# Performance work log

Measured on AMD Instinct MI355X. Metric: run time of the kernel, lower is better.

The kernel has to match this reference:

```python
import jax, jax.numpy as jnp
import numpy as np
from jax import lax

B, T = 32, 256
VOCAB, WDIM, MDIM = 50000, 300, 50
HID, NLAYERS, NCLASSES = 512, 2, 3


def _init(key, shape, scale):
    return (jax.random.normal(key, shape, dtype=jnp.float32) * scale)


def setup_inputs() -> dict:
    key = jax.random.key(0)
    ks = jax.random.split(key, 20)
    inputs_seq = jax.random.randint(ks[0], (B, T), 0, VOCAB, dtype=jnp.int32)
    masks = jax.random.randint(ks[1], (B, T), 0, 2, dtype=jnp.int32)
    length = jax.random.randint(ks[2], (B, 1), T // 2, T + 1, dtype=jnp.int32)
    embedding = _init(ks[3], (VOCAB, WDIM), 0.1)
    mask_embedding = _init(ks[4], (2, MDIM), 0.1)
    transition = _init(ks[5], (2, 2), 1.0)
    d_in0 = WDIM + MDIM          # 350
    d_in1 = 2 * HID              # 1024
    w_fw0 = _init(ks[6], (d_in0 + HID, 4 * HID), 0.02)
    b_fw0 = jnp.zeros((4 * HID,), jnp.float32)
    w_bw0 = _init(ks[7], (d_in0 + HID, 4 * HID), 0.02)
    b_bw0 = jnp.zeros((4 * HID,), jnp.float32)
    w_fw1 = _init(ks[8], (d_in1 + HID, 4 * HID), 0.02)
    b_fw1 = jnp.zeros((4 * HID,), jnp.float32)
    w_bw1 = _init(ks[9], (d_in1 + HID, 4 * HID), 0.02)
    b_bw1 = jnp.zeros((4 * HID,), jnp.float32)
    crf_w = _init(ks[10], (2 * HID, 2), 0.02)
    crf_b = jnp.zeros((2,), jnp.float32)
    logits_w = _init(ks[11], (2 * HID, NCLASSES), 0.02)
    logits_b = jnp.zeros((NCLASSES,), jnp.float32)
    return dict(inputs_seq=inputs_seq, masks=masks, length=length,
                embedding=embedding, mask_embedding=mask_embedding,
                transition=transition,
                w_fw0=w_fw0, b_fw0=b_fw0, w_bw0=w_bw0, b_bw0=b_bw0,
                w_fw1=w_fw1, b_fw1=b_fw1, w_bw1=w_bw1, b_bw1=b_bw1,
                crf_w=crf_w, crf_b=crf_b, logits_w=logits_w, logits_b=logits_b)


def _lstm_scan(x, length, W, b):
    """TF LSTMCell (gate order i, j, f, o; forget_bias=1.0) over time.
    Outputs are zeroed and state held past sequence_length (dynamic_rnn semantics)."""
    Bb, Tt, _ = x.shape
    H = W.shape[1] // 4
    zero = jnp.zeros((Bb, H), x.dtype)

    def step(carry, inp):
        h, c = carry
        xt, t = inp
        z = jnp.concatenate([xt, h], axis=-1) @ W + b
        i, j, f, o = jnp.split(z, 4, axis=-1)
        c_new = jax.nn.sigmoid(f + 1.0) * c + jax.nn.sigmoid(i) * jnp.tanh(j)
        h_new = jax.nn.sigmoid(o) * jnp.tanh(c_new)
        m = (t < length)[:, None]
        c = jnp.where(m, c_new, c)
        h = jnp.where(m, h_new, h)
        out = jnp.where(m, h_new, 0.0)
        return (h, c), out

    _, ys = lax.scan(step, (zero, zero), (x.transpose(1, 0, 2), jnp.arange(Tt)))
    return ys.transpose(1, 0, 2)  # [B,T,H]


def _reverse_seq(x, length):
    """tf.reverse_sequence along time: reverse first `length` steps, keep rest."""
    Tt = x.shape[1]
    t = jnp.arange(Tt)[None, :]
    L = length[:, None]
    idx = jnp.where(t < L, L - 1 - t, t)  # [B,T]
    return jnp.take_along_axis(x, idx[:, :, None], axis=1)


def _forward(inputs_seq, masks, length, embedding, mask_embedding, transition,
             lstm_params, crf_w, crf_b, logits_w, logits_b):
    length = length.reshape(-1)  # tf.squeeze
    emb = embedding[inputs_seq]          # [B,T,WDIM]
    memb = mask_embedding[masks]         # [B,T,MDIM]
    out = jnp.concatenate([emb, memb], axis=-1)
    for (wf, bf, wb, bb) in lstm_params:
        fw = _lstm_scan(out, length, wf, bf)
        bw = _reverse_seq(_lstm_scan(_reverse_seq(out, length), length, wb, bb), length)
        out = jnp.concatenate([fw, bw], axis=-1)  # [B,T,2H]

    # CRF forward probabilities over 2 tags
    e = out @ crf_w + crf_b              # [B,T,2] emission scores
    Tt = e.shape[1]
    alpha0 = e[:, 0]

    def crf_step(alpha, inp):
        et, t = inp
        new = jax.nn.logsumexp(alpha[:, :, None] + transition[None], axis=1) + et
        m = (t < length)[:, None]
        alpha = jnp.where(m, new, alpha)
        p = jnp.where(m, jax.nn.softmax(alpha, axis=-1), 0.0)
        return alpha, p

    _, probs_rest = lax.scan(crf_step, alpha0,
                             (e[:, 1:].transpose(1, 0, 2), jnp.arange(1, Tt)))
    p0 = jnp.where((length > 0)[:, None], jax.nn.softmax(alpha0, axis=-1), 0.0)
    probs = jnp.concatenate([p0[None], probs_rest], axis=0).transpose(1, 0, 2)  # [B,T,2]

    crf_out = probs[:, :, -1][:, None, :]            # [B,1,T]
    sentiment_vector = crf_out @ out                  # [B,1,2H]
    logits = jax.nn.softmax(sentiment_vector @ logits_w + logits_b, axis=-1)
    return logits  # [B,1,NCLASSES]


def reference(inputs_seq, masks, length, embedding, mask_embedding, transition,
              w_fw0, b_fw0, w_bw0, b_bw0, w_fw1, b_fw1, w_bw1, b_bw1,
              crf_w, crf_b, logits_w, logits_b):
    lstm_params = [(w_fw0, b_fw0, w_bw0, b_bw0), (w_fw1, b_fw1, w_bw1, b_bw1)]
    return _forward(inputs_seq, masks, length, embedding, mask_embedding,
                    transition, lstm_params, crf_w, crf_b, logits_w, logits_b)
```

## Files before the change

kernel.cpp:

```cpp
#include <hip/hip_runtime.h>
#include <hip/hip_bf16.h>
#include <cstdint>
#include <cstddef>

#define BB 32
#define TT 256
#define HID 512

typedef __attribute__((ext_vector_type(8))) short short8v;
typedef __attribute__((ext_vector_type(4))) float float4v;
typedef __attribute__((ext_vector_type(4))) unsigned int uint4v;

__device__ __forceinline__ float bf2f(unsigned short u) {
  return __uint_as_float(((unsigned int)u) << 16);
}
__device__ __forceinline__ unsigned short f2bf(float f) {
  unsigned int x = __float_as_uint(f);
  x += 0x7fffu + ((x >> 16) & 1u);
  return (unsigned short)(x >> 16);
}

__device__ __forceinline__ void stg1_cohere(float* p, float v) {
  asm volatile("global_store_dword %0, %1, off sc0 sc1"
               :: "v"(p), "v"(v) : "memory");
}
__device__ __forceinline__ void ldg4u_cohere_issue(uint4v& d, const unsigned short* p) {
  asm volatile("global_load_dwordx4 %0, %1, off sc0 sc1"
               : "=v"(d) : "v"(p) : "memory");
}
__device__ __forceinline__ void wait_vm0() {
  asm volatile("s_waitcnt vmcnt(0)" ::: "memory");
  __builtin_amdgcn_sched_barrier(0);
}

__global__ __launch_bounds__(256) void prep_all(
    const float* __restrict__ w_fw0, const float* __restrict__ w_bw0,
    const float* __restrict__ w_fw1, const float* __restrict__ w_bw1,
    unsigned short* __restrict__ wxt0f, unsigned short* __restrict__ wxt0b,
    unsigned short* __restrict__ wxt1f, unsigned short* __restrict__ wxt1b,
    unsigned short* __restrict__ whT0f, unsigned short* __restrict__ whT0b,
    unsigned short* __restrict__ whT1f, unsigned short* __restrict__ whT1b,
    const int* __restrict__ ids, const int* __restrict__ msk,
    const float* __restrict__ emb, const float* __restrict__ memb,
    unsigned short* __restrict__ x0b,
    float* __restrict__ zero_base)
{
  __shared__ float tile[64][65];
  int blk = blockIdx.x;
  int tid = threadIdx.x;
  if (blk < 2432) {
    const float* W; unsigned short* dst; int Kreal, Kpad, base;
    if (blk < 192)       { W = w_fw0; dst = wxt0f; Kreal = 350;  Kpad = 384;  base = 0; }
    else if (blk < 384)  { W = w_bw0; dst = wxt0b; Kreal = 350;  Kpad = 384;  base = 192; }
    else if (blk < 896)  { W = w_fw1; dst = wxt1f; Kreal = 1024; Kpad = 1024; base = 384; }
    else if (blk < 1408) { W = w_bw1; dst = wxt1b; Kreal = 1024; Kpad = 1024; base = 896; }
    else if (blk < 1664) { W = w_fw0 + (size_t)350 * 2048;  dst = whT0f; Kreal = 512; Kpad = 512; base = 1408; }
    else if (blk < 1920) { W = w_bw0 + (size_t)350 * 2048;  dst = whT0b; Kreal = 512; Kpad = 512; base = 1664; }
    else if (blk < 2176) { W = w_fw1 + (size_t)1024 * 2048; dst = whT1f; Kreal = 512; Kpad = 512; base = 1920; }
    else                 { W = w_bw1 + (size_t)1024 * 2048; dst = whT1b; Kreal = 512; Kpad = 512; base = 2176; }
    int rel = blk - base;
    int n0 = (rel & 31) * 64;
    int k0 = (rel >> 5) * 64;
#pragma unroll
    for (int i = 0; i < 4; ++i) {
      int e = tid + 256 * i;
      int r = e >> 4, c4 = (e & 15) * 4;
      float4 v = make_float4(0.f, 0.f, 0.f, 0.f);
      if (k0 + r < Kreal) v = *(const float4*)(W + (size_t)(k0 + r) * 2048 + n0 + c4);
      tile[r][c4 + 0] = v.x; tile[r][c4 + 1] = v.y;
      tile[r][c4 + 2] = v.z; tile[r][c4 + 3] = v.w;
    }
    __syncthreads();
    int nl = tid >> 2;
    int kg = (tid & 3) * 16;
    unsigned int pk[4], pk2[4];
#pragma unroll
    for (int jj = 0; jj < 4; ++jj) {
      unsigned short lo = f2bf(tile[kg + jj * 2 + 0][nl]);
      unsigned short hi = f2bf(tile[kg + jj * 2 + 1][nl]);
      pk[jj] = (unsigned int)lo | ((unsigned int)hi << 16);
    }
#pragma unroll
    for (int jj = 0; jj < 4; ++jj) {
      unsigned short lo = f2bf(tile[kg + 8 + jj * 2 + 0][nl]);
      unsigned short hi = f2bf(tile[kg + 8 + jj * 2 + 1][nl]);
      pk2[jj] = (unsigned int)lo | ((unsigned int)hi << 16);
    }
    size_t off = (size_t)(n0 + nl) * Kpad + k0 + kg;
    *(uint4*)(dst + off) = make_uint4(pk[0], pk[1], pk[2], pk[3]);
    *(uint4*)(dst + off + 8) = make_uint4(pk2[0], pk2[1], pk2[2], pk2[3]);
  } else if (blk < 3456) {
    int r = blk - 2432;
    int bt = r * 8 + (tid >> 5);
    int id = ids[bt];
    int m  = msk[bt];
    const float* er = emb  + (size_t)id * 300;
    const float* mr = memb + (size_t)m * 50;
    for (int d = tid & 31; d < 384; d += 32) {
      float v = (d < 300) ? er[d] : (d < 350 ? mr[d - 300] : 0.f);
      x0b[(size_t)bt * 384 + d] = f2bf(v);
    }
  } else {
    int r = blk - 3456;
    float4* p = (float4*)zero_base + (size_t)r * 1280 + tid;
#pragma unroll
    for (int i = 0; i < 5; ++i) p[i * 256] = make_float4(0.f, 0.f, 0.f, 0.f);
  }
}

__global__ __launch_bounds__(256) void gemm_xproj2(
    const unsigned short* __restrict__ A,
    const unsigned short* __restrict__ wxtF, const unsigned short* __restrict__ wxtB,
    const float* __restrict__ biasF, const float* __restrict__ biasB,
    unsigned short* __restrict__ xqF, unsigned short* __restrict__ xqB,
    int Kpad, int nkb)
{
  __shared__ unsigned short ws_s[128 * 64];
  __shared__ unsigned short xs_s[32 * 64];
  __shared__ float bias_s[128];
  int z = blockIdx.z;
  const unsigned short* wxt = z ? wxtB : wxtF;
  const float* bias = z ? biasB : biasF;
  unsigned short* xq = z ? xqB : xqF;
  int tid = threadIdx.x;
  int lane = tid & 63;
  int w = tid >> 6;
  int pos = blockIdx.x;
  int n0 = blockIdx.y * 128;
  if (tid < 128) bias_s[tid] = bias[n0 + tid];

  float4v acc[2][2];
#pragma unroll
  for (int i = 0; i < 2; ++i)
#pragma unroll
    for (int j = 0; j < 2; ++j) acc[i][j] = (float4v)0.f;

  int brow = tid >> 3;
  int seg = tid & 7;
  for (int kb = 0; kb < nkb; ++kb) {
    int k0 = kb * 64;
    __syncthreads();
    {
      const unsigned short* src = A + (size_t)(brow * 256 + pos) * Kpad + k0 + seg * 8;
      uint4 v = *(const uint4*)src;
      int o = (brow * 128 + seg * 16) ^ ((brow & 7) << 4);
      *(uint4*)((char*)xs_s + o) = v;
    }
#pragma unroll
    for (int i = 0; i < 4; ++i) {
      int n = i * 32 + brow;
      const unsigned short* src = wxt + (size_t)(n0 + n) * Kpad + k0 + seg * 8;
      uint4 v = *(const uint4*)src;
      int o = (n * 128 + seg * 16) ^ ((n & 7) << 4);
      *(uint4*)((char*)ws_s + o) = v;
    }
    __syncthreads();
#pragma unroll
    for (int kin = 0; kin < 64; kin += 32) {
      int kl = kin + ((lane >> 4) << 3);
      short8v afrag[2], bfrag[2];
#pragma unroll
      for (int nt = 0; nt < 2; ++nt) {
        int nl = w * 32 + nt * 16 + (lane & 15);
        int o = (nl * 128 + kl * 2) ^ ((nl & 7) << 4);
        afrag[nt] = *(const short8v*)((const char*)ws_s + o);
      }
#pragma unroll
      for (int bt = 0; bt < 2; ++bt) {
        int bl = bt * 16 + (lane & 15);
        int o = (bl * 128 + kl * 2) ^ ((bl & 7) << 4);
        bfrag[bt] = *(const short8v*)((const char*)xs_s + o);
      }
#pragma unroll
      for (int nt = 0; nt < 2; ++nt)
#pragma unroll
        for (int bt = 0; bt < 2; ++bt)
          acc[nt][bt] = __builtin_amdgcn_mfma_f32_16x16x32_bf16(
              afrag[nt], bfrag[bt], acc[nt][bt], 0, 0, 0);
    }
  }
  unsigned short* outp = xq + (size_t)pos * 65536;
#pragma unroll
  for (int nt = 0; nt < 2; ++nt) {
#pragma unroll
    for (int bt = 0; bt < 2; ++bt) {
#pragma unroll
      for (int reg = 0; reg < 4; ++reg) {
        int nl = w * 32 + nt * 16 + ((lane >> 4) << 2) + reg;
        int b = bt * 16 + (lane & 15);
        float v = acc[nt][bt][reg] + bias_s[nl];
        outp[(size_t)(n0 + nl) * 32 + b] = f2bf(v);
      }
    }
  }
}

__global__ __launch_bounds__(256) void lstm_mfma(
    const unsigned short* __restrict__ xq_fw, const unsigned short* __restrict__ xq_bw,
    const unsigned short* __restrict__ whT_fw, const unsigned short* __restrict__ whT_bw,
    const int* __restrict__ length,
    unsigned short* __restrict__ out,
    unsigned short* __restrict__ hT,
    float* __restrict__ cbuf,
    int* __restrict__ flags,
    int t0, int t1)
{
  extern __shared__ char smem[];
  float* zs = (float*)(smem + 65536);
  unsigned short* hb_st = (unsigned short*)(smem + 69632);
  unsigned short* ob_st = (unsigned short*)(smem + 70144);
  int tid = threadIdx.x;
  int wg = blockIdx.x;
  int dir = wg >> 6;
  int widx = wg & 63;
  int u0 = widx << 3;
  const unsigned short* xq = dir ? xq_bw : xq_fw;
  const unsigned short* whT = dir ? whT_bw : whT_fw;
  unsigned short* hbase = hT + (size_t)dir * 32768;
  int* dirflags = flags + dir * 2048;
  int* myflag = dirflags + widx * 32;

  {
    int r = tid >> 3;
    int q = r >> 3, d = r & 7;
    const unsigned short* src = whT + (size_t)(q * 512 + u0 + d) * 512 + (tid & 7) * 8;
    int ob = r * 1024 + (tid & 7) * 16;
    int sw = (r & 7) << 4;
#pragma unroll
    for (int i = 0; i < 8; ++i) {
      uint4 v = *(const uint4*)(src + i * 64);
      *(uint4*)(smem + ((ob + i * 128) ^ sw)) = v;
    }
  }

  int lane = tid & 63;
  int w = tid >> 6;
  int wr = w >> 1, wc = w & 1;
  int arow = wr * 16 + (lane & 15);
  int bcol = wc * 16 + (lane & 15);
  int chunk16 = (lane >> 4) << 4;
  int asw = (arow & 7) << 4;
  int bsw = (bcol & 7) << 4;
  int fu = tid >> 5;
  int fb = tid & 31;
  int ug = u0 + fu;
  int L = length[fb];
  float creg = 0.f;

  for (int t = t0; t < t1; ++t) {
    int sl = dir ? (TT - 1 - t) : t;
    const unsigned short* hTr_g = hbase + (size_t)(t & 1) * 16384;
    unsigned short* hTw_g = hbase + (size_t)((t & 1) ^ 1) * 16384;

    const unsigned short* xr = xq + (size_t)sl * 65536 + (size_t)ug * 32 + fb;
    float xv0 = bf2f(xr[0]);
    float xv1 = bf2f(xr[16384]);
    float xv2 = bf2f(xr[32768]);
    float xv3 = bf2f(xr[49152]);

    {
      int row = tid >> 3;
      int ob = 32768 + row * 1024 + (tid & 7) * 16;
      int sw = (row & 7) << 4;
      if (t == 0) {
        uint4v zv = (uint4v)0u;
#pragma unroll
        for (int i = 0; i < 8; ++i)
          *(uint4v*)(smem + ((ob + i * 128) ^ sw)) = zv;
      } else {
        const unsigned short* src = hTr_g + row * 512 + (tid & 7) * 8;
        uint4v r0, r1, r2, r3, r4, r5, r6, r7;
        ldg4u_cohere_issue(r0, src + 0 * 64);
        ldg4u_cohere_issue(r1, src + 1 * 64);
        ldg4u_cohere_issue(r2, src + 2 * 64);
        ldg4u_cohere_issue(r3, src + 3 * 64);
        ldg4u_cohere_issue(r4, src + 4 * 64);
        ldg4u_cohere_issue(r5, src + 5 * 64);
        ldg4u_cohere_issue(r6, src + 6 * 64);
        ldg4u_cohere_issue(r7, src + 7 * 64);
        wait_vm0();
        *(uint4v*)(smem + ((ob + 0 * 128) ^ sw)) = r0;
        *(uint4v*)(smem + ((ob + 1 * 128) ^ sw)) = r1;
        *(uint4v*)(smem + ((ob + 2 * 128) ^ sw)) = r2;
        *(uint4v*)(smem + ((ob + 3 * 128) ^ sw)) = r3;
        *(uint4v*)(smem + ((ob + 4 * 128) ^ sw)) = r4;
        *(uint4v*)(smem + ((ob + 5 * 128) ^ sw)) = r5;
        *(uint4v*)(smem + ((ob + 6 * 128) ^ sw)) = r6;
        *(uint4v*)(smem + ((ob + 7 * 128) ^ sw)) = r7;
      }
    }
    __syncthreads();

    float4v acc = (float4v)0.f;
#pragma unroll
    for (int ks = 0; ks < 16; ++ks) {
      int kb = ks * 64 + chunk16;
      short8v af = *(const short8v*)(smem + (size_t)arow * 1024 + (kb ^ asw));
      short8v bf = *(const short8v*)(smem + 32768 + (size_t)bcol * 1024 + (kb ^ bsw));
      acc = __builtin_amdgcn_mfma_f32_16x16x32_bf16(af, bf, acc, 0, 0, 0);
    }
#pragma unroll
    for (int r = 0; r < 4; ++r) {
      int row = wr * 16 + ((lane >> 4) << 2) + r;
      zs[row * 32 + bcol] = acc[r];
    }
    __syncthreads();

    {
      bool active = sl < L;
      float z0 = zs[(0 * 8 + fu) * 32 + fb] + xv0;
      float z1 = zs[(1 * 8 + fu) * 32 + fb] + xv1;
      float z2 = zs[(2 * 8 + fu) * 32 + fb] + xv2;
      float z3 = zs[(3 * 8 + fu) * 32 + fb] + xv3;
      int ho = 32768 + fb * 1024 + ((ug * 2) ^ ((fb & 7) << 4));
      float h_old = bf2f(*(const unsigned short*)(smem + ho));
      float c_old = cbuf ? ((t > 0) ? cbuf[dir * 16384 + ug * 32 + fb] : 0.f) : creg;
      float si = 1.f / (1.f + expf(-z0));
      float sj = tanhf(z1);
      float sf = 1.f / (1.f + expf(-(z2 + 1.f)));
      float so = 1.f / (1.f + expf(-z3));
      float cn = sf * c_old + si * sj;
      float hn = so * tanhf(cn);
      if (active) {
        if (cbuf) cbuf[dir * 16384 + ug * 32 + fb] = cn; else creg = cn;
      }
      hb_st[fb * 8 + fu] = f2bf(active ? hn : h_old);
      ob_st[fb * 8 + fu] = f2bf(active ? hn : 0.f);
    }
    __syncthreads();

    if (tid < 32) {
      uint4v hv = *(const uint4v*)(hb_st + tid * 8);
      asm volatile("global_store_dwordx4 %0, %1, off sc0 sc1"
                   :: "v"(hTw_g + tid * 512 + u0), "v"(hv) : "memory");
      uint4v ov = *(const uint4v*)(ob_st + tid * 8);
      *(uint4v*)(out + (size_t)(tid * TT + sl) * 1024 + dir * 512 + u0) = ov;
    }

    if (t1 - t0 > 1) {
      wait_vm0();
      __syncthreads();
      if (tid == 0) {
        __hip_atomic_store(myflag, t + 1, __ATOMIC_RELAXED,
                           __HIP_MEMORY_SCOPE_AGENT);
      }
      if (tid < 64) {
        int* f = dirflags + tid * 32;
        while (__hip_atomic_load(f, __ATOMIC_RELAXED,
                                 __HIP_MEMORY_SCOPE_AGENT) < t + 1) {
          __builtin_amdgcn_s_sleep(1);
        }
      }
      __syncthreads();
    }
  }
}

__global__ __launch_bounds__(256) void crf_final(
    const unsigned short* __restrict__ out1,
    const float* __restrict__ crf_w, const float* __restrict__ crf_b,
    const float* __restrict__ trans,
    const int* __restrict__ length,
    const float* __restrict__ lw, const float* __restrict__ lb,
    float* __restrict__ dout)
{
  __shared__ float e[TT][2];
  __shared__ float pw[TT];
  __shared__ float sv[1024];
  __shared__ float red[256];
  int b = blockIdx.x, tid = threadIdx.x;
  int lane = tid & 63, w = tid >> 6;
  const unsigned short* ob = out1 + (size_t)b * TT * 1024;
  for (int t = w; t < TT; t += 4) {
    float a0 = 0.f, a1 = 0.f;
    for (int i = 0; i < 16; ++i) {
      int d = lane + i * 64;
      float v = bf2f(ob[(size_t)t * 1024 + d]);
      a0 += v * crf_w[d * 2];
      a1 += v * crf_w[d * 2 + 1];
    }
    for (int off = 32; off; off >>= 1) {
      a0 += __shfl_down(a0, off);
      a1 += __shfl_down(a1, off);
    }
    if (lane == 0) { e[t][0] = a0 + crf_b[0]; e[t][1] = a1 + crf_b[1]; }
  }
  __syncthreads();
  if (tid == 0) {
    int L = length[b];
    float t00 = trans[0], t01 = trans[1], t10 = trans[2], t11 = trans[3];
    float a0 = e[0][0], a1 = e[0][1];
    {
      float m = fmaxf(a0, a1);
      float e0 = expf(a0 - m), e1 = expf(a1 - m);
      pw[0] = (L > 0) ? (e1 / (e0 + e1)) : 0.f;
    }
    for (int t = 1; t < TT; ++t) {
      if (t < L) {
        float x0 = a0 + t00, y0 = a1 + t10;
        float m0 = fmaxf(x0, y0);
        float n0 = m0 + logf(expf(x0 - m0) + expf(y0 - m0)) + e[t][0];
        float x1 = a0 + t01, y1 = a1 + t11;
        float m1 = fmaxf(x1, y1);
        float n1 = m1 + logf(expf(x1 - m1) + expf(y1 - m1)) + e[t][1];
        a0 = n0; a1 = n1;
        float m = fmaxf(a0, a1);
        float e0 = expf(a0 - m), e1 = expf(a1 - m);
        pw[t] = e1 / (e0 + e1);
      } else {
        pw[t] = 0.f;
      }
    }
  }
  __syncthreads();
  for (int i = 0; i < 4; ++i) {
    int d = tid + i * 256;
    float s = 0.f;
    for (int t = 0; t < TT; ++t) s += pw[t] * bf2f(ob[(size_t)t * 1024 + d]);
    sv[d] = s;
  }
  __syncthreads();
  float v[3];
  for (int c = 0; c < 3; ++c) {
    float s = 0.f;
    for (int i = 0; i < 4; ++i) {
      int d = tid + i * 256;
      s += sv[d] * lw[d * 3 + c];
    }
    red[tid] = s;
    __syncthreads();
    for (int off = 128; off; off >>= 1) {
      if (tid < off) red[tid] += red[tid + off];
      __syncthreads();
    }
    if (tid == 0) v[c] = red[0] + lb[c];
    __syncthreads();
  }
  if (tid == 0) {
    float m = fmaxf(v[0], fmaxf(v[1], v[2]));
    float e0 = expf(v[0] - m), e1 = expf(v[1] - m), e2 = expf(v[2] - m);
    float s = e0 + e1 + e2;
    dout[b * 3 + 0] = e0 / s;
    dout[b * 3 + 1] = e1 / s;
    dout[b * 3 + 2] = e2 / s;
  }
}

#define LSTM_LDS 70656

static void run_layer(const unsigned short* xq_fw, const unsigned short* xq_bw,
                      const unsigned short* whT_fw, const unsigned short* whT_bw,
                      const int* len, unsigned short* out, unsigned short* hT,
                      float* cbuf_, int* flags, hipStream_t stream) {
  const unsigned short* a0 = xq_fw; const unsigned short* a1 = xq_bw;
  const unsigned short* a2 = whT_fw; const unsigned short* a3 = whT_bw;
  const int* a4 = len; unsigned short* a5 = out; unsigned short* a6 = hT;
  float* a7 = nullptr; int* a8 = flags; int a9 = 0, a10 = TT;
  void* args[11] = { &a0, &a1, &a2, &a3, &a4, &a5, &a6, &a7, &a8, &a9, &a10 };
  hipError_t err = hipLaunchCooperativeKernel(
      reinterpret_cast<const void*>(lstm_mfma), dim3(128), dim3(256),
      args, LSTM_LDS, stream);
  if (err != hipSuccess) {
    for (int t = 0; t < TT; ++t) {
      lstm_mfma<<<128, 256, LSTM_LDS, stream>>>(
          xq_fw, xq_bw, whT_fw, whT_bw, len, out, hT, cbuf_, flags, t, t + 1);
    }
  }
}

extern "C" void kernel_launch(void* const* d_in, const int* in_sizes, int n_in,
                              void* d_out, int out_size, void* d_ws, size_t ws_size,
                              hipStream_t stream) {
  (void)in_sizes; (void)n_in; (void)out_size; (void)ws_size;
  const int* ids    = (const int*)d_in[0];
  const int* msk    = (const int*)d_in[1];
  const int* len    = (const int*)d_in[2];
  const float* emb  = (const float*)d_in[3];
  const float* memb = (const float*)d_in[4];
  const float* trans= (const float*)d_in[5];
  const float* w_fw0= (const float*)d_in[6];
  const float* b_fw0= (const float*)d_in[7];
  const float* w_bw0= (const float*)d_in[8];
  const float* b_bw0= (const float*)d_in[9];
  const float* w_fw1= (const float*)d_in[10];
  const float* b_fw1= (const float*)d_in[11];
  const float* w_bw1= (const float*)d_in[12];
  const float* b_bw1= (const float*)d_in[13];
  const float* crf_w= (const float*)d_in[14];
  const float* crf_b= (const float*)d_in[15];
  const float* lw   = (const float*)d_in[16];
  const float* lb   = (const float*)d_in[17];
  float* outp = (float*)d_out;

  float* ws = (float*)d_ws;
  unsigned short* x0b   = (unsigned short*)(ws);
  unsigned short* wxt0f = (unsigned short*)(ws + 1572864);
  unsigned short* wxt0b = (unsigned short*)(ws + 1966080);
  unsigned short* wxt1f = (unsigned short*)(ws + 2359296);
  unsigned short* wxt1b = (unsigned short*)(ws + 3407872);
  unsigned short* whT0f = (unsigned short*)(ws + 4456448);
  unsigned short* whT0b = (unsigned short*)(ws + 4980736);
  unsigned short* whT1f = (unsigned short*)(ws + 5505024);
  unsigned short* whT1b = (unsigned short*)(ws + 6029312);
  unsigned short* xqf   = (unsigned short*)(ws + 6553600);
  unsigned short* xqb   = (unsigned short*)(ws + 14942208);
  unsigned short* out0b = (unsigned short*)(ws + 23330816);
  unsigned short* out1b = (unsigned short*)(ws + 27525120);
  unsigned short* hT    = (unsigned short*)(ws + 31719424);
  float* cbuf_ = ws + 31752192;
  int*   flagsA = (int*)(ws + 31784960);
  int*   flagsB = (int*)(ws + 31789056);

  (void)hipFuncSetAttribute(reinterpret_cast<const void*>(lstm_mfma),
                            hipFuncAttributeMaxDynamicSharedMemorySize, LSTM_LDS);

  prep_all<<<3464, 256, 0, stream>>>(
      w_fw0, w_bw0, w_fw1, w_bw1,
      wxt0f, wxt0b, wxt1f, wxt1b,
      whT0f, whT0b, whT1f, whT1b,
      ids, msk, emb, memb, x0b, cbuf_);

  gemm_xproj2<<<dim3(256, 16, 2), 256, 0, stream>>>(
      x0b, wxt0f, wxt0b, b_fw0, b_bw0, xqf, xqb, 384, 6);

  run_layer(xqf, xqb, whT0f, whT0b, len, out0b, hT, cbuf_, flagsA, stream);

  gemm_xproj2<<<dim3(256, 16, 2), 256, 0, stream>>>(
      out0b, wxt1f, wxt1b, b_fw1, b_bw1, xqf, xqb, 1024, 16);

  run_layer(xqf, xqb, whT1f, whT1b, len, out1b, hT, cbuf_, flagsB, stream);

  crf_final<<<32, 256, 0, stream>>>(out1b, crf_w, crf_b, trans, len, lw, lb, outp);
}
```

Before: 2.086 ms.

## Trim LSTM step latency: fast math, x prefetch, lighter inter-block barrier

Replaces precise expf/tanhf in the LSTM cell and CRF with __expf-based sigmoid/tanh approximations. Prefetches the next timestep's input-projection values before the cross-block flag wait so their latency overlaps the spin. Moves the output store to a different wavefront and drops one __syncthreads by letting only the first wave wait on its stores before publishing the flag. This targets per-timestep serial latency in the persistent recurrent kernel, at the cost of slightly lower accuracy in the activations. The flag is now published after only that wave's stores complete, so the out stores issued by another wave are no longer covered by the wait.

```diff
diff --git a/kernel.cpp b/kernel.cpp
--- a/kernel.cpp
+++ b/kernel.cpp
@@ -19,11 +19,13 @@
   x += 0x7fffu + ((x >> 16) & 1u);
   return (unsigned short)(x >> 16);
 }
-
-__device__ __forceinline__ void stg1_cohere(float* p, float v) {
-  asm volatile("global_store_dword %0, %1, off sc0 sc1"
-               :: "v"(p), "v"(v) : "memory");
-}
+__device__ __forceinline__ float fsig(float x) {
+  return 1.f / (1.f + __expf(-x));
+}
+__device__ __forceinline__ float ftanh(float x) {
+  return 1.f - 2.f / (__expf(2.f * x) + 1.f);
+}
+
 __device__ __forceinline__ void ldg4u_cohere_issue(uint4v& d, const unsigned short* p) {
   asm volatile("global_load_dwordx4 %0, %1, off sc0 sc1"
                : "=v"(d) : "v"(p) : "memory");
@@ -247,16 +249,21 @@
   int L = length[fb];
   float creg = 0.f;
 
+  const unsigned short* xbase = xq + (size_t)ug * 32 + fb;
+  float xv0, xv1, xv2, xv3;
+  {
+    int sl0 = dir ? (TT - 1 - t0) : t0;
+    const unsigned short* xr = xbase + (size_t)sl0 * 65536;
+    xv0 = bf2f(xr[0]);
+    xv1 = bf2f(xr[16384]);
+    xv2 = bf2f(xr[32768]);
+    xv3 = bf2f(xr[49152]);
+  }
+
   for (int t = t0; t < t1; ++t) {
     int sl = dir ? (TT - 1 - t) : t;
     const unsigned short* hTr_g = hbase + (size_t)(t & 1) * 16384;
     unsigned short* hTw_g = hbase + (size_t)((t & 1) ^ 1) * 16384;
-
-    const unsigned short* xr = xq + (size_t)sl * 65536 + (size_t)ug * 32 + fb;
-    float xv0 = bf2f(xr[0]);
-    float xv1 = bf2f(xr[16384]);
-    float xv2 = bf2f(xr[32768]);
-    float xv3 = bf2f(xr[49152]);
 
     {
       int row = tid >> 3;
@@ -315,12 +322,12 @@
       int ho = 32768 + fb * 1024 + ((ug * 2) ^ ((fb & 7) << 4));
       float h_old = bf2f(*(const unsigned short*)(smem + ho));
       float c_old = cbuf ? ((t > 0) ? cbuf[dir * 16384 + ug * 32 + fb] : 0.f) : creg;
-      float si = 1.f / (1.f + expf(-z0));
-      float sj = tanhf(z1);
-      float sf = 1.f / (1.f + expf(-(z2 + 1.f)));
-      float so = 1.f / (1.f + expf(-z3));
+      float si = fsig(z0);
+      float sj = ftanh(z1);
+      float sf = fsig(z2 + 1.f);
+      float so = fsig(z3);
       float cn = sf * c_old + si * sj;
-      float hn = so * tanhf(cn);
+      float hn = so * ftanh(cn);
       if (active) {
         if (cbuf) cbuf[dir * 16384 + ug * 32 + fb] = cn; else creg = cn;
       }
@@ -333,18 +340,29 @@
       uint4v hv = *(const uint4v*)(hb_st + tid * 8);
       asm volatile("global_store_dwordx4 %0, %1, off sc0 sc1"
                    :: "v"(hTw_g + tid * 512 + u0), "v"(hv) : "memory");
-      uint4v ov = *(const uint4v*)(ob_st + tid * 8);
-      *(uint4v*)(out + (size_t)(tid * TT + sl) * 1024 + dir * 512 + u0) = ov;
+    } else if (tid >= 64 && tid < 96) {
+      int b = tid - 64;
+      uint4v ov = *(const uint4v*)(ob_st + b * 8);
+      *(uint4v*)(out + (size_t)(b * TT + sl) * 1024 + dir * 512 + u0) = ov;
+    }
+
+    float nxv0 = 0.f, nxv1 = 0.f, nxv2 = 0.f, nxv3 = 0.f;
+    if (t + 1 < t1) {
+      int sl2 = dir ? (TT - 2 - t) : (t + 1);
+      const unsigned short* xr = xbase + (size_t)sl2 * 65536;
+      nxv0 = bf2f(xr[0]);
+      nxv1 = bf2f(xr[16384]);
+      nxv2 = bf2f(xr[32768]);
+      nxv3 = bf2f(xr[49152]);
     }
 
     if (t1 - t0 > 1) {
-      wait_vm0();
-      __syncthreads();
-      if (tid == 0) {
-        __hip_atomic_store(myflag, t + 1, __ATOMIC_RELAXED,
-                           __HIP_MEMORY_SCOPE_AGENT);
-      }
       if (tid < 64) {
+        wait_vm0();
+        if (tid == 0) {
+          __hip_atomic_store(myflag, t + 1, __ATOMIC_RELAXED,
+                             __HIP_MEMORY_SCOPE_AGENT);
+        }
         int* f = dirflags + tid * 32;
         while (__hip_atomic_load(f, __ATOMIC_RELAXED,
                                  __HIP_MEMORY_SCOPE_AGENT) < t + 1) {
@@ -353,6 +371,7 @@
       }
       __syncthreads();
     }
+    xv0 = nxv0; xv1 = nxv1; xv2 = nxv2; xv3 = nxv3;
   }
 }
 
@@ -392,20 +411,20 @@
     float a0 = e[0][0], a1 = e[0][1];
     {
       float m = fmaxf(a0, a1);
-      float e0 = expf(a0 - m), e1 = expf(a1 - m);
+      float e0 = __expf(a0 - m), e1 = __expf(a1 - m);
       pw[0] = (L > 0) ? (e1 / (e0 + e1)) : 0.f;
     }
     for (int t = 1; t < TT; ++t) {
       if (t < L) {
         float x0 = a0 + t00, y0 = a1 + t10;
         float m0 = fmaxf(x0, y0);
-        float n0 = m0 + logf(expf(x0 - m0) + expf(y0 - m0)) + e[t][0];
+        float n0 = m0 + __logf(__expf(x0 - m0) + __expf(y0 - m0)) + e[t][0];
         float x1 = a0 + t01, y1 = a1 + t11;
         float m1 = fmaxf(x1, y1);
-        float n1 = m1 + logf(expf(x1 - m1) + expf(y1 - m1)) + e[t][1];
+        float n1 = m1 + __logf(__expf(x1 - m1) + __expf(y1 - m1)) + e[t][1];
         a0 = n0; a1 = n1;
         float m = fmaxf(a0, a1);
-        float e0 = expf(a0 - m), e1 = expf(a1 - m);
+        float e0 = __expf(a0 - m), e1 = __expf(a1 - m);
         pw[t] = e1 / (e0 + e1);
       } else {
         pw[t] = 0.f;
@@ -438,7 +457,7 @@
   }
   if (tid == 0) {
     float m = fmaxf(v[0], fmaxf(v[1], v[2]));
-    float e0 = expf(v[0] - m), e1 = expf(v[1] - m), e2 = expf(v[2] - m);
+    float e0 = __expf(v[0] - m), e1 = __expf(v[1] - m), e2 = __expf(v[2] - m);
     float s = e0 + e1 + e2;
     dout[b * 3 + 0] = e0 / s;
     dout[b * 3 + 1] = e1 / s;
```

New measurement: 2.004 ms. -3.9%, faster.
